# Optimization experiments

Measured on AMD Instinct MI355X. Metric: run time of the kernel, lower is better.

## Reference

```python
import jax, jax.numpy as jnp
import numpy as np

B, N, D, F, OUT = 2048, 784, 10, 2, 10
EPS = 1e-12


def setup_inputs() -> dict:
    key = jax.random.key(0)
    k1, k2, k3, k4 = jax.random.split(key, 4)
    x = jax.random.uniform(k1, (B, N), dtype=jnp.float32)  # pixel values in [0,1]
    # xavier-uniform-like init matching the torch module's std formulas
    std0 = (2.0 / (F + F * D)) ** 0.5
    core0 = jax.random.uniform(k2, (1, F, D), jnp.float32, -std0, std0)
    stdm = (2.0 / (D * F + F * D)) ** 0.5
    cores_mid = jax.random.uniform(k3, (N - 1, D, F, D), jnp.float32, -stdm, stdm)
    classifier = jax.random.normal(k4, (OUT, D), jnp.float32) * 0.1
    return {"x": x, "core0": core0, "cores_mid": cores_mid, "classifier": classifier}


def reference(x, core0, cores_mid, classifier):
    Bsz = x.shape[0]
    xf = x.reshape(Bsz, -1)                      # [B, N]
    feats = jnp.stack([1.0 - xf, xf], axis=-1)   # [B, N, F] feature map

    # per-site contraction of cores with features (all sites at once)
    head = jnp.einsum('ldh,bd->blh', core0, feats[:, 0])            # [B, 1, D]
    tail = jnp.einsum('nldh,bnd->bnlh', cores_mid, feats[:, 1:])    # [B, N-1, D, D]

    log_norm = jnp.zeros(Bsz, dtype=x.dtype)
    # log-depth binary tree contraction; shapes shrink by ~half each level
    # (static shapes per level -> Python while is jit-compatible)
    while tail.shape[1] > 0:
        # pair 0: head (left-boundary tensor) with next tensor
        nh = head @ tail[:, 0]                                      # [B, 1, D]
        hn = jnp.maximum(jnp.sqrt(jnp.sum(nh * nh, axis=(-2, -1))), EPS)
        log_norm = log_norm + jnp.log(hn)
        head = nh / hn[:, None, None]
        # remaining tensors paired (t1,t2),(t3,t4),... ; odd leftover is carried
        rest = tail[:, 1:]
        p = rest.shape[1] // 2
        a = rest[:, 0:2 * p:2]                                      # [B, p, D, D]
        b = rest[:, 1:2 * p:2]                                      # [B, p, D, D]
        c = a @ b                                                   # [B, p, D, D]
        norms = jnp.maximum(jnp.sqrt(jnp.sum(c * c, axis=(-2, -1))), EPS)  # [B, p]
        log_norm = log_norm + jnp.sum(jnp.log(norms), axis=1)
        c = c / norms[..., None, None]
        tail = jnp.concatenate([c, rest[:, 2 * p:]], axis=1)
    mps_output = head[:, 0]                                         # [B, D]
    logits = mps_output @ classifier.T + log_norm[:, None]          # [B, OUT]
    return logits
```

## Files before the change

kernel.cpp:

```cpp
#include <hip/hip_runtime.h>


constexpr int Bsz = 2048;
constexpr int Nn  = 784;
constexpr int NS  = 783;
constexpr int LCH = 16;
constexpr int NCH = (NS + LCH - 1) / LCH;

#define PKH_FMA(d, a, b, c) \
  asm("v_pk_fma_f16 %0, %1, %2, %3" : "=v"(d) : "v"(a), "v"(b), "v"(c))
#define PKH_ACC_LO(d, m, s) \
  asm("v_pk_fma_f16 %0, %1, %2, %0 op_sel:[0,0,0] op_sel_hi:[1,0,1]" \
      : "+v"(d) : "v"(m), "v"(s))
#define PKH_ACC_HI(d, m, s) \
  asm("v_pk_fma_f16 %0, %1, %2, %0 op_sel:[0,1,0] op_sel_hi:[1,1,1]" \
      : "+v"(d) : "v"(m), "v"(s))
#define PKH_MUL_LO(d, m, s) \
  asm("v_pk_mul_f16 %0, %1, %2 op_sel:[0,0] op_sel_hi:[1,0]" \
      : "=v"(d) : "v"(m), "v"(s))
#define CVT_H2F(f, u) asm("v_cvt_f32_f16 %0, %1" : "=v"(f) : "v"(u))

__device__ __forceinline__ unsigned short f2h_bits(float f) {
    union { _Float16 h; unsigned short u; } c;
    c.h = (_Float16)f;
    return c.u;
}
__device__ __forceinline__ float hlo(unsigned u) {
    union { unsigned short s; _Float16 h; } c;
    c.s = (unsigned short)(u & 0xffff);
    return (float)c.h;
}
__device__ __forceinline__ float hhi(unsigned u) {
    union { unsigned short s; _Float16 h; } c;
    c.s = (unsigned short)(u >> 16);
    return (float)c.h;
}

__global__ __launch_bounds__(256, 4) void chunk_kernel(
    const float* __restrict__ x, const float* __restrict__ cores,
    unsigned* __restrict__ pbuf, float* __restrict__ lbuf) {
    __shared__ unsigned s_w[LCH * 100];
    __shared__ float    s_x[128 * 17];

    const int c   = blockIdx.y;
    const int n0  = 1 + c * LCH;
    const int n1  = min(n0 + LCH, Nn);
    const int ns  = n1 - n0;
    const int tid = (int)threadIdx.x;
    const int b0  = (int)blockIdx.x * 128;

    for (int e = tid; e < ns * 50; e += 256) {
        const int k = e / 50, s = e - k * 50;
        const int i = s / 5, q = s - i * 5;
        const float* g = cores + (size_t)(n0 - 1 + k) * 200 + i * 20 + 2 * q;
        const float a0 = g[0], a1 = g[1], bb0 = g[10], bb1 = g[11];
        const unsigned A = ((unsigned)f2h_bits(2.f * a1) << 16) | f2h_bits(2.f * a0);
        const unsigned D = ((unsigned)f2h_bits(2.f * (bb1 - a1)) << 16) |
                           f2h_bits(2.f * (bb0 - a0));
        s_w[k * 100 + 2 * s]     = A;
        s_w[k * 100 + 2 * s + 1] = D;
    }
    for (int e = tid; e < 128 * 16; e += 256) {
        const int bl = e >> 4, k = e & 15;
        if (k < ns) s_x[bl * 17 + k] = x[(size_t)(b0 + bl) * Nn + n0 + k];
    }
    __syncthreads();

    const int h = tid & 1;
    const int u = tid >> 1;
    const int b = b0 + u;
    const float* __restrict__ xs = s_x + u * 17;

    unsigned p[5][5];
    {
        const unsigned short xb = f2h_bits(xs[0]);
        const unsigned x2 = ((unsigned)xb << 16) | xb;
#pragma unroll
        for (int r = 0; r < 5; ++r)
#pragma unroll
            for (int q = 0; q < 5; ++q) {
                const unsigned A = s_w[(5 * h + r) * 10 + 2 * q];
                const unsigned D = s_w[(5 * h + r) * 10 + 2 * q + 1];
                PKH_FMA(p[r][q], D, x2, A);
            }
    }

    for (int k = 1; k < ns; ++k) {
        const unsigned short xb = f2h_bits(xs[k]);
        const unsigned x2 = ((unsigned)xb << 16) | xb;
        const unsigned* ws = s_w + k * 100;

        unsigned Mf[50];
#pragma unroll
        for (int ip = 0; ip < 5; ++ip) {
            const uint4* w4 = (const uint4*)(ws + ip * 20);
#pragma unroll
            for (int t = 0; t < 5; ++t) {
                const uint4 w = w4[t];
                PKH_FMA(Mf[ip * 10 + 2 * t],     w.y, x2, w.x);
                PKH_FMA(Mf[ip * 10 + 2 * t + 1], w.w, x2, w.z);
            }
        }

#pragma unroll
        for (int r = 0; r < 5; ++r) {
            unsigned acc[5];
#pragma unroll
            for (int q = 0; q < 5; ++q)
                PKH_MUL_LO(acc[q], Mf[q], p[r][0]);
#pragma unroll
            for (int q = 0; q < 5; ++q)
                PKH_ACC_HI(acc[q], Mf[5 + q], p[r][0]);
#pragma unroll
            for (int ip = 1; ip < 5; ++ip) {
#pragma unroll
                for (int q = 0; q < 5; ++q)
                    PKH_ACC_LO(acc[q], Mf[ip * 10 + q], p[r][ip]);
#pragma unroll
                for (int q = 0; q < 5; ++q)
                    PKH_ACC_HI(acc[q], Mf[ip * 10 + 5 + q], p[r][ip]);
            }
#pragma unroll
            for (int q = 0; q < 5; ++q) p[r][q] = acc[q];
        }
    }

    float ss = 0.f;
#pragma unroll
    for (int r = 0; r < 5; ++r)
#pragma unroll
        for (int q = 0; q < 5; ++q) {
            const float lo = hlo(p[r][q]), hi = hhi(p[r][q]);
            ss = fmaf(lo, lo, ss);
            ss = fmaf(hi, hi, ss);
        }
    ss += __shfl_xor(ss, 1);
    ss = fmaxf(ss, 1e-30f);
    const float rin = rsqrtf(ss);
    if (h == 0)
        lbuf[(size_t)c * Bsz + b] = 0.5f * __logf(ss) - (float)ns * 0.69314718056f;

    unsigned* dst = pbuf + ((size_t)c * Bsz + b) * 50;
#pragma unroll
    for (int r = 0; r < 5; ++r)
#pragma unroll
        for (int q = 0; q < 5; ++q) {
            const float lo = hlo(p[r][q]) * rin;
            const float hi = hhi(p[r][q]) * rin;
            dst[(5 * h + r) * 5 + q] =
                ((unsigned)f2h_bits(hi) << 16) | f2h_bits(lo);
        }
}

__global__ __launch_bounds__(64, 1) void combine_kernel(
    const float* __restrict__ x, const float* __restrict__ core0,
    const float* __restrict__ cls, const unsigned* __restrict__ pbuf,
    const float* __restrict__ lbuf, float* __restrict__ out, int C) {
    __shared__ __align__(16) unsigned ring[8][256];

    const int tid   = (int)threadIdx.x;
    const int j     = tid & 15;
    const int jj    = (j < 10) ? j : 9;
    const int gbase = tid & 48;
    const int sl    = tid >> 4;
    const int b     = (int)blockIdx.x * 4 + sl;
    const int qoff  = jj >> 1;
    const unsigned sh = (unsigned)(jj & 1) * 16;

    float v[10];
    const float x0 = x[(size_t)b * Nn];
#pragma unroll
    for (int i = 0; i < 10; ++i) {
        const float c0 = core0[i], c1 = core0[10 + i];
        v[i] = fmaf(x0, c1 - c0, c0);
    }
    float llog = 0.f;
    for (int cc = j; cc < C; cc += 16)
        llog += lbuf[(size_t)cc * Bsz + b];
    llog += __shfl_xor(llog, 1);
    llog += __shfl_xor(llog, 2);
    llog += __shfl_xor(llog, 4);
    llog += __shfl_xor(llog, 8);

    const int flat = (tid * 4 <= 196) ? tid * 4 : 196;
    const unsigned* gsrc0 = pbuf + (size_t)blockIdx.x * 200 + flat;
    const size_t cstride = (size_t)Bsz * 50;

#define STAGE(cc)                                                          \
    __builtin_amdgcn_global_load_lds(                                      \
        (const __attribute__((address_space(1))) unsigned*)(gsrc0 +        \
            (size_t)(cc) * cstride),                                       \
        (__attribute__((address_space(3))) unsigned*)&ring[(cc) & 7][0],   \
        16, 0, 0)

#pragma unroll
    for (int d = 0; d < 7; ++d) STAGE(d);

    const int lbase = sl * 50 + qoff;
    for (int c = 0; c < C; ++c) {
        const int d = c & 7;
        if (c + 7 <= C - 1) {
            asm volatile("s_waitcnt vmcnt(6)" ::: "memory");
        } else {
            asm volatile("s_waitcnt vmcnt(0)" ::: "memory");
        }
        __builtin_amdgcn_sched_barrier(0);

        float acc = 0.f;
#pragma unroll
        for (int i = 0; i < 10; ++i) {
            unsigned ud = ring[d][lbase + i * 5] >> sh;
            float wv;
            CVT_H2F(wv, ud);
            acc = fmaf(v[i], wv, acc);
        }
        if (j >= 10) acc = 0.f;
        if ((c & 7) == 7 || c == C - 1) {
            float s = acc * acc;
            s += __shfl_xor(s, 1);
            s += __shfl_xor(s, 2);
            s += __shfl_xor(s, 4);
            s += __shfl_xor(s, 8);
            s = fmaxf(s, 1e-30f);
            llog += 0.5f * __logf(s);
            acc *= rsqrtf(s);
        }
#pragma unroll
        for (int i = 0; i < 10; ++i) v[i] = __shfl(acc, gbase + i);

        if (c + 7 < C) STAGE(c + 7);
    }
#undef STAGE

    if (j < 10) {
        float acc = llog;
#pragma unroll
        for (int i = 0; i < 10; ++i) acc = fmaf(v[i], cls[j * 10 + i], acc);
        out[(size_t)b * 10 + j] = acc;
    }
}

extern "C" void kernel_launch(void* const* d_in, const int* in_sizes, int n_in,
                              void* d_out, int out_size, void* d_ws, size_t ws_size,
                              hipStream_t stream) {
    const float* x     = (const float*)d_in[0];
    const float* core0 = (const float*)d_in[1];
    const float* cores = (const float*)d_in[2];
    const float* cls   = (const float*)d_in[3];
    float* out = (float*)d_out;

    const int C = NCH;
    unsigned* pbuf = (unsigned*)d_ws;
    float*    lbuf = (float*)(pbuf + (size_t)C * Bsz * 50);

    hipLaunchKernelGGL(chunk_kernel, dim3(Bsz / 128, C), dim3(256),
                       0, stream, x, cores, pbuf, lbuf);
    hipLaunchKernelGGL(combine_kernel, dim3(Bsz / 4), dim3(64),
                       0, stream, x, core0, cls, pbuf, lbuf, out, C);
}
```

Baseline: 72.58 us.

## Halve chunk length and pair-multiply chunk matrices in the combine kernel

```diff
diff --git a/kernel.cpp b/kernel.cpp
--- a/kernel.cpp
+++ b/kernel.cpp
@@ -4,7 +4,7 @@
 constexpr int Bsz = 2048;
 constexpr int Nn  = 784;
 constexpr int NS  = 783;
-constexpr int LCH = 16;
+constexpr int LCH = 8;
 constexpr int NCH = (NS + LCH - 1) / LCH;
 
 #define PKH_FMA(d, a, b, c) \
@@ -40,7 +40,7 @@
     const float* __restrict__ x, const float* __restrict__ cores,
     unsigned* __restrict__ pbuf, float* __restrict__ lbuf) {
     __shared__ unsigned s_w[LCH * 100];
-    __shared__ float    s_x[128 * 17];
+    __shared__ float    s_x[128 * 9];
 
     const int c   = blockIdx.y;
     const int n0  = 1 + c * LCH;
@@ -60,16 +60,16 @@
         s_w[k * 100 + 2 * s]     = A;
         s_w[k * 100 + 2 * s + 1] = D;
     }
-    for (int e = tid; e < 128 * 16; e += 256) {
-        const int bl = e >> 4, k = e & 15;
-        if (k < ns) s_x[bl * 17 + k] = x[(size_t)(b0 + bl) * Nn + n0 + k];
+    for (int e = tid; e < 128 * 8; e += 256) {
+        const int bl = e >> 3, k = e & 7;
+        if (k < ns) s_x[bl * 9 + k] = x[(size_t)(b0 + bl) * Nn + n0 + k];
     }
     __syncthreads();
 
     const int h = tid & 1;
     const int u = tid >> 1;
     const int b = b0 + u;
-    const float* __restrict__ xs = s_x + u * 17;
+    const float* __restrict__ xs = s_x + u * 9;
 
     unsigned p[5][5];
     {
@@ -156,7 +156,7 @@
     const float* __restrict__ x, const float* __restrict__ core0,
     const float* __restrict__ cls, const unsigned* __restrict__ pbuf,
     const float* __restrict__ lbuf, float* __restrict__ out, int C) {
-    __shared__ __align__(16) unsigned ring[8][256];
+    __shared__ __align__(16) unsigned ring[16][256];
 
     const int tid   = (int)threadIdx.x;
     const int j     = tid & 15;
@@ -190,32 +190,66 @@
     __builtin_amdgcn_global_load_lds(                                      \
         (const __attribute__((address_space(1))) unsigned*)(gsrc0 +        \
             (size_t)(cc) * cstride),                                       \
-        (__attribute__((address_space(3))) unsigned*)&ring[(cc) & 7][0],   \
+        (__attribute__((address_space(3))) unsigned*)&ring[(cc) & 15][0],  \
         16, 0, 0)
 
 #pragma unroll
-    for (int d = 0; d < 7; ++d) STAGE(d);
-
-    const int lbase = sl * 50 + qoff;
-    for (int c = 0; c < C; ++c) {
-        const int d = c & 7;
-        if (c + 7 <= C - 1) {
-            asm volatile("s_waitcnt vmcnt(6)" ::: "memory");
+    for (int d = 0; d < 12; ++d) STAGE(d);
+
+    const int P = C / 2;
+    const int lbase = sl * 50;
+
+    for (int pc = 0; pc < P; ++pc) {
+        if (pc <= (C - 12) / 2) {
+            asm volatile("s_waitcnt vmcnt(10)" ::: "memory");
         } else {
             asm volatile("s_waitcnt vmcnt(0)" ::: "memory");
         }
         __builtin_amdgcn_sched_barrier(0);
 
+        const int dA = (2 * pc) & 15;
+        const int dB = (2 * pc + 1) & 15;
+
+        unsigned P1d[50];
+        {
+            const uint4* p1q = (const uint4*)&ring[dA][lbase];
+#pragma unroll
+            for (int g = 0; g < 12; ++g) {
+                const uint4 w = p1q[g];
+                P1d[4 * g]     = w.x;
+                P1d[4 * g + 1] = w.y;
+                P1d[4 * g + 2] = w.z;
+                P1d[4 * g + 3] = w.w;
+            }
+            P1d[48] = ring[dA][lbase + 48];
+            P1d[49] = ring[dA][lbase + 49];
+        }
+        unsigned p2p[10];
+#pragma unroll
+        for (int k = 0; k < 10; ++k) p2p[k] = ring[dB][lbase + k * 5 + qoff];
+
+        unsigned e[10];
+#pragma unroll
+        for (int i = 0; i < 10; ++i) {
+            PKH_MUL_LO(e[i], p2p[0], P1d[i * 5]);
+            PKH_ACC_HI(e[i], p2p[1], P1d[i * 5]);
+#pragma unroll
+            for (int t = 1; t < 5; ++t) {
+                PKH_ACC_LO(e[i], p2p[2 * t],     P1d[i * 5 + t]);
+                PKH_ACC_HI(e[i], p2p[2 * t + 1], P1d[i * 5 + t]);
+            }
+        }
+
         float acc = 0.f;
 #pragma unroll
         for (int i = 0; i < 10; ++i) {
-            unsigned ud = ring[d][lbase + i * 5] >> sh;
+            const unsigned ud = e[i] >> sh;
             float wv;
             CVT_H2F(wv, ud);
             acc = fmaf(v[i], wv, acc);
         }
         if (j >= 10) acc = 0.f;
-        if ((c & 7) == 7 || c == C - 1) {
+        if ((pc & 3) == 3 || pc == P - 1) {
             float s = acc * acc;
             s += __shfl_xor(s, 1);
             s += __shfl_xor(s, 2);
@@ -228,7 +262,8 @@
 #pragma unroll
         for (int i = 0; i < 10; ++i) v[i] = __shfl(acc, gbase + i);
 
-        if (c + 7 < C) STAGE(c + 7);
+        if (2 * pc + 12 < C) STAGE(2 * pc + 12);
+        if (2 * pc + 13 < C) STAGE(2 * pc + 13);
     }
 #undef STAGE
 
```

Result: slower. 120.4 us (+65.9%).
